# Performance work log

Hardware: AMD Instinct MI355X
Metric: run time of the kernel (lower is better)

Reference implementation:

```python
import jax, jax.numpy as jnp
import numpy as np
from jax.ops import segment_sum

N_NODES = 100000
N_EDGES = 1600000
N_GRAPHS = 64
IN_DIM = 128
HID = 128
N_CLASSES = 10


def setup_inputs() -> dict:
    key = jax.random.key(0)
    ks = jax.random.split(key, 8)
    h = jax.random.normal(ks[0], (N_NODES, IN_DIM), dtype=jnp.float32)
    src = jax.random.randint(ks[1], (N_EDGES,), 0, N_NODES, dtype=jnp.int64)
    dst = jax.random.randint(ks[2], (N_EDGES,), 0, N_NODES, dtype=jnp.int64)
    graph_ids = jnp.sort(jax.random.randint(ks[3], (N_NODES,), 0, N_GRAPHS, dtype=jnp.int64))
    # Glorot-ish scaled weights
    W1 = jax.random.normal(ks[4], (IN_DIM, HID), dtype=jnp.float32) / np.sqrt(IN_DIM)
    b1 = jnp.zeros((HID,), dtype=jnp.float32)
    W2 = jax.random.normal(ks[5], (HID, HID), dtype=jnp.float32) / np.sqrt(HID)
    b2 = jnp.zeros((HID,), dtype=jnp.float32)
    Wc = jax.random.normal(ks[6], (HID, N_CLASSES), dtype=jnp.float32) / np.sqrt(HID)
    bc = jnp.zeros((N_CLASSES,), dtype=jnp.float32)
    return {"h": h, "src": src, "dst": dst, "graph_ids": graph_ids,
            "W1": W1, "b1": b1, "W2": W2, "b2": b2, "Wc": Wc, "bc": bc}


def _graph_conv(h, src, dst, W, b, n_nodes):
    # DGL GraphConv, norm='both': D_out^{-1/2} scaling of src feats,
    # sum aggregation over edges, D_in^{-1/2} scaling of dst, then XW + b.
    ones = jnp.ones((src.shape[0],), dtype=h.dtype)
    deg_out = jnp.clip(segment_sum(ones, src, num_segments=n_nodes), 1.0)
    deg_in = jnp.clip(segment_sum(ones, dst, num_segments=n_nodes), 1.0)
    hn = h * jax.lax.rsqrt(deg_out)[:, None]          # [N, d]
    agg = segment_sum(hn[src], dst, num_segments=n_nodes)  # SpMM: [N, d]
    agg = agg * jax.lax.rsqrt(deg_in)[:, None]
    return agg @ W + b


def reference(h, src, dst, graph_ids, W1, b1, W2, b2, Wc, bc):
    n = h.shape[0]
    x = jax.nn.relu(_graph_conv(h, src, dst, W1, b1, n))
    x = jax.nn.relu(_graph_conv(x, src, dst, W2, b2, n))
    # mean_nodes readout per graph
    counts = jnp.clip(segment_sum(jnp.ones((n,), x.dtype), graph_ids, num_segments=N_GRAPHS), 1.0)
    hg = segment_sum(x, graph_ids, num_segments=N_GRAPHS) / counts[:, None]  # [G, d]
    return hg @ Wc + bc  # [G, n_classes]
```

## Files before the change

### kernel.cpp

```cpp
#include <hip/hip_runtime.h>

#define DIM 128
#define NG 64
#define NCLS 10
#define CAP 64
#define WSZ 256
#define NWMAX 512
#define CAPB 8192
#define EPB 8192
#define HL 4
#define WTP 68

typedef __attribute__((ext_vector_type(8))) short s8v;
typedef __attribute__((ext_vector_type(4))) float f4v;

__device__ inline unsigned short f2bf(float f) {
    unsigned int u = __float_as_uint(f);
    unsigned int r = (u + 0x7fffu + ((u >> 16) & 1u)) >> 16;
    return (unsigned short)r;
}
__device__ inline unsigned int pack2bf(float a, float b) {
    return ((unsigned int)f2bf(b) << 16) | (unsigned int)f2bf(a);
}

__global__ void prep_kernel(const float* __restrict__ W1, const float* __restrict__ W2,
                            unsigned short* __restrict__ Wt1, unsigned short* __restrict__ Wt2,
                            int* curD, int* curS, uint4* hb4, uint4* x1b4, int nw, int n) {
    int t = blockIdx.x * 256 + threadIdx.x;
    if (t < nw) {
        curD[t] = t * CAPB;
        curS[t] = t * CAPB;
    }
    if (t < 32768) {
        int which = t >> 14;
        int i = t & 16383;
        int c = i >> 7, k = i & 127;
        (which ? Wt2 : Wt1)[i] = f2bf((which ? W2 : W1)[k * 128 + c]);
    }
    if (t < 16) {
        uint4 z = make_uint4(0, 0, 0, 0);
        hb4[(size_t)n * 16 + t] = z;
        x1b4[(size_t)n * 16 + t] = z;
    }
}

__global__ __launch_bounds__(256) void bucket_kernel(const int* __restrict__ src,
                                                     const int* __restrict__ dst,
                                                     int* curD, int* curS,
                                                     int* __restrict__ bucketD,
                                                     unsigned char* __restrict__ bucketS,
                                                     int e, int nw) {
    __shared__ int histD[NWMAX];
    __shared__ int histS[NWMAX];
    int t = threadIdx.x;
    for (int i = t; i < nw; i += 256) { histD[i] = 0; histS[i] = 0; }
    __syncthreads();
    int lo = blockIdx.x * EPB;
    int hi = min(e, lo + EPB);
    for (int i = lo + t * 4; i < hi; i += 1024) {
        int4 d4 = *(const int4*)&dst[i];
        int4 s4 = *(const int4*)&src[i];
        atomicAdd(&histD[d4.x >> 8], 1); atomicAdd(&histS[s4.x >> 8], 1);
        atomicAdd(&histD[d4.y >> 8], 1); atomicAdd(&histS[s4.y >> 8], 1);
        atomicAdd(&histD[d4.z >> 8], 1); atomicAdd(&histS[s4.z >> 8], 1);
        atomicAdd(&histD[d4.w >> 8], 1); atomicAdd(&histS[s4.w >> 8], 1);
    }
    __syncthreads();
    for (int i = t; i < nw; i += 256) {
        int hd = histD[i], hs = histS[i];
        histD[i] = hd ? atomicAdd(&curD[i], hd) : 0;
        histS[i] = hs ? atomicAdd(&curS[i], hs) : 0;
    }
    __syncthreads();
    for (int i = lo + t * 4; i < hi; i += 1024) {
        int4 d4 = *(const int4*)&dst[i];
        int4 s4 = *(const int4*)&src[i];
#pragma unroll
        for (int j = 0; j < 4; ++j) {
            int d = (&d4.x)[j], s = (&s4.x)[j];
            int sd = atomicAdd(&histD[d >> 8], 1);
            bucketD[sd] = (s << 8) | (d & 255);
            int ss = atomicAdd(&histS[s >> 8], 1);
            bucketS[ss] = (unsigned char)(s & 255);
        }
    }
}

__global__ __launch_bounds__(256) void window_kernel(const int* __restrict__ curD,
                                                     const int* __restrict__ curS,
                                                     const int* __restrict__ bucketD,
                                                     const unsigned char* __restrict__ bucketS,
                                                     const float* __restrict__ h,
                                                     int* __restrict__ cnt_in,
                                                     float* __restrict__ rs_in,
                                                     float* __restrict__ rs_out,
                                                     int* __restrict__ colx_pad,
                                                     uint4* __restrict__ hb4, int n) {
    __shared__ int cin[WSZ];
    __shared__ int cout[WSZ];
    __shared__ float rsO_s[WSZ];
    int w = blockIdx.x, t = threadIdx.x;
    cin[t] = 0;
    cout[t] = 0;
    __syncthreads();
    int base = w * CAPB;
    int nE = min(curD[w] - base, CAPB);
    for (int i = t; i < nE; i += 256) {
        int v = bucketD[base + i];
        int d8 = v & 255;
        int slot = atomicAdd(&cin[d8], 1);
        if (slot < CAP) colx_pad[(((w << 8) + d8) << 6) + slot] = v >> 8;
    }
    int nS = min(curS[w] - base, CAPB);
    for (int i = t; i < nS; i += 256) atomicAdd(&cout[bucketS[base + i]], 1);
    __syncthreads();
    int node = (w << 8) + t;
    if (node < n) {
        int c = cin[t];
        cnt_in[node] = c;
        rs_in[node] = rsqrtf(fmaxf((float)c, 1.0f));
        float ro = rsqrtf(fmaxf((float)cout[t], 1.0f));
        rs_out[node] = ro;
        rsO_s[t] = ro;
        int cc = min(c, CAP);
        int c4 = min((cc + 3) & ~3, CAP);
        for (int s = cc; s < c4; ++s) colx_pad[((size_t)node << 6) + s] = n;
    }
    __syncthreads();
    for (int idx = t; idx < WSZ * 16; idx += 256) {
        int rl = idx >> 4, sub = idx & 15;
        int nd = (w << 8) + rl;
        if (nd < n) {
            float s = rsO_s[rl];
            float4 a = ((const float4*)h)[(size_t)nd * 32 + sub * 2];
            float4 b = ((const float4*)h)[(size_t)nd * 32 + sub * 2 + 1];
            uint4 o;
            o.x = pack2bf(a.x * s, a.y * s);
            o.y = pack2bf(a.z * s, a.w * s);
            o.z = pack2bf(b.x * s, b.y * s);
            o.w = pack2bf(b.z * s, b.w * s);
            hb4[(size_t)nd * 16 + sub] = o;
        }
    }
}

__global__ __launch_bounds__(256) void spmm_bf16(const uint4* __restrict__ xb4,
                                                 const int* __restrict__ cnt_in,
                                                 const int* __restrict__ colx_pad,
                                                 const float* __restrict__ rs_in,
                                                 uint4* __restrict__ yb4, int n) {
    int node = (blockIdx.x * 256 + threadIdx.x) >> 6;
    int lane = threadIdx.x & 63;
    if (node >= n) return;
    int g = lane >> 4, sub = lane & 15;
    int cnt = min(cnt_in[node], CAP);
    int cnt4 = min((cnt + 3) & ~3, CAP);
    int myc = colx_pad[((size_t)node << 6) + ((lane < cnt4) ? lane : 0)];
    float acc[8] = {0.f, 0.f, 0.f, 0.f, 0.f, 0.f, 0.f, 0.f};
    int j = 0;
    for (; j + 16 <= cnt4; j += 16) {
        uint4 v[4];
#pragma unroll
        for (int b = 0; b < 4; ++b) {
            int c = __shfl(myc, j + 4 * b + g);
            v[b] = xb4[(size_t)c * 16 + sub];
        }
#pragma unroll
        for (int b = 0; b < 4; ++b) {
            acc[0] += __uint_as_float(v[b].x << 16);
            acc[1] += __uint_as_float(v[b].x & 0xffff0000u);
            acc[2] += __uint_as_float(v[b].y << 16);
            acc[3] += __uint_as_float(v[b].y & 0xffff0000u);
            acc[4] += __uint_as_float(v[b].z << 16);
            acc[5] += __uint_as_float(v[b].z & 0xffff0000u);
            acc[6] += __uint_as_float(v[b].w << 16);
            acc[7] += __uint_as_float(v[b].w & 0xffff0000u);
        }
    }
    for (; j < cnt4; j += 4) {
        int c = __shfl(myc, j + g);
        uint4 v = xb4[(size_t)c * 16 + sub];
        acc[0] += __uint_as_float(v.x << 16);
        acc[1] += __uint_as_float(v.x & 0xffff0000u);
        acc[2] += __uint_as_float(v.y << 16);
        acc[3] += __uint_as_float(v.y & 0xffff0000u);
        acc[4] += __uint_as_float(v.z << 16);
        acc[5] += __uint_as_float(v.z & 0xffff0000u);
        acc[6] += __uint_as_float(v.w << 16);
        acc[7] += __uint_as_float(v.w & 0xffff0000u);
    }
#pragma unroll
    for (int i = 0; i < 8; ++i) {
        acc[i] += __shfl_xor(acc[i], 16);
        acc[i] += __shfl_xor(acc[i], 32);
    }
    if (g == 0) {
        float w = rs_in[node];
        uint4 o;
        o.x = pack2bf(acc[0] * w, acc[1] * w);
        o.y = pack2bf(acc[2] * w, acc[3] * w);
        o.z = pack2bf(acc[4] * w, acc[5] * w);
        o.w = pack2bf(acc[6] * w, acc[7] * w);
        yb4[(size_t)node * 16 + sub] = o;
    }
}

__device__ inline void stage_wt(const uint4* __restrict__ Wt4, unsigned int* WtL, int t) {
#pragma unroll
    for (int i = 0; i < 8; ++i) {
        int q = t + 256 * i;
        int row = q >> 4, col4 = q & 15;
        *(uint4*)&WtL[row * WTP + col4 * 4] = Wt4[q];
    }
}

__global__ __launch_bounds__(256) void mm_mfma(const unsigned char* __restrict__ A,
                                               const uint4* __restrict__ Wt4,
                                               const float* __restrict__ bias,
                                               const float* __restrict__ rs_out,
                                               unsigned short* __restrict__ out, int n) {
    __shared__ unsigned int WtL[128 * WTP];
    int t = threadIdx.x;
    stage_wt(Wt4, WtL, t);
    int wave = t >> 6, lane = t & 63;
    int m = lane & 15, q = lane >> 4;
    int r0 = (int)blockIdx.x * 64 + wave * 16;
    int arow = min(r0 + m, n - 1);
    __syncthreads();
    f4v acc[8];
#pragma unroll
    for (int c = 0; c < 8; ++c) acc[c] = (f4v){0.f, 0.f, 0.f, 0.f};
#pragma unroll
    for (int k0 = 0; k0 < 4; ++k0) {
        s8v a = *(const s8v*)(A + (size_t)arow * 256 + k0 * 64 + q * 16);
#pragma unroll
        for (int c = 0; c < 8; ++c) {
            s8v b = *(const s8v*)&WtL[(c * 16 + m) * WTP + k0 * 16 + q * 4];
            acc[c] = __builtin_amdgcn_mfma_f32_16x16x32_bf16(a, b, acc[c], 0, 0, 0);
        }
    }
#pragma unroll
    for (int c = 0; c < 8; ++c) {
        float bv = bias[c * 16 + m];
#pragma unroll
        for (int r = 0; r < 4; ++r) {
            int row = r0 + q * 4 + r;
            if (row < n) {
                float val = fmaxf(acc[c][r] + bv, 0.0f);
                out[(size_t)row * 128 + c * 16 + m] = f2bf(val * rs_out[row]);
            }
        }
    }
}

__global__ __launch_bounds__(256) void mm_mfma_readout(const unsigned char* __restrict__ A,
                                                       const uint4* __restrict__ Wt4,
                                                       const float* __restrict__ bias,
                                                       const int* __restrict__ gid,
                                                       float* __restrict__ hg, int n) {
    __shared__ unsigned int WtL[128 * WTP];
    __shared__ float hgloc[HL][DIM];
    int t = threadIdx.x;
    stage_wt(Wt4, WtL, t);
    for (int i = t; i < HL * DIM; i += 256) ((float*)hgloc)[i] = 0.0f;
    int wave = t >> 6, lane = t & 63;
    int m = lane & 15, q = lane >> 4;
    int r0 = (int)blockIdx.x * 64 + wave * 16;
    int b0 = (int)blockIdx.x * 64;
    int gid0 = gid[min(b0, n - 1)];
    int arow = min(r0 + m, n - 1);
    __syncthreads();
    f4v acc[8];
#pragma unroll
    for (int c = 0; c < 8; ++c) acc[c] = (f4v){0.f, 0.f, 0.f, 0.f};
#pragma unroll
    for (int k0 = 0; k0 < 4; ++k0) {
        s8v a = *(const s8v*)(A + (size_t)arow * 256 + k0 * 64 + q * 16);
#pragma unroll
        for (int c = 0; c < 8; ++c) {
            s8v b = *(const s8v*)&WtL[(c * 16 + m) * WTP + k0 * 16 + q * 4];
            acc[c] = __builtin_amdgcn_mfma_f32_16x16x32_bf16(a, b, acc[c], 0, 0, 0);
        }
    }
    int gfirst = gid[min(r0, n - 1)];
    int glast = gid[min(r0 + 15, n - 1)];
    bool uni = (gfirst == glast) && (r0 + 15 < n);
    if (uni) {
        int gl = gfirst - gid0;
#pragma unroll
        for (int c = 0; c < 8; ++c) {
            float bv = bias[c * 16 + m];
            float s = fmaxf(acc[c][0] + bv, 0.0f) + fmaxf(acc[c][1] + bv, 0.0f) +
                      fmaxf(acc[c][2] + bv, 0.0f) + fmaxf(acc[c][3] + bv, 0.0f);
            s += __shfl_xor(s, 16);
            s += __shfl_xor(s, 32);
            if (q == 0) {
                if (gl < HL)
                    atomicAdd(&hgloc[gl][c * 16 + m], s);
                else
                    atomicAdd(&hg[(size_t)gfirst * DIM + c * 16 + m], s);
            }
        }
    } else {
#pragma unroll
        for (int r = 0; r < 4; ++r) {
            int row = r0 + q * 4 + r;
            if (row < n) {
                int g = gid[row];
                int gl = g - gid0;
#pragma unroll
                for (int c = 0; c < 8; ++c) {
                    float val = fmaxf(acc[c][r] + bias[c * 16 + m], 0.0f);
                    if (gl < HL)
                        atomicAdd(&hgloc[gl][c * 16 + m], val);
                    else
                        atomicAdd(&hg[(size_t)g * DIM + c * 16 + m], val);
                }
            }
        }
    }
    __syncthreads();
    for (int i = t; i < HL * DIM; i += 256) {
        float v = ((float*)hgloc)[i];
        int g = gid0 + (i >> 7);
        if (v != 0.0f && g < NG) atomicAdd(&hg[(size_t)g * DIM + (i & 127)], v);
    }
}

__global__ void classify_kernel(const float* __restrict__ hg, const int* __restrict__ gid,
                                const float* __restrict__ Wc, const float* __restrict__ bc,
                                float* __restrict__ out, int n) {
    __shared__ float inv;
    int g = blockIdx.x, t = threadIdx.x;
    if (t == 0) {
        int lo = 0, hi = n;
        while (lo < hi) { int mid = (lo + hi) >> 1; if (gid[mid] < g) lo = mid + 1; else hi = mid; }
        int lb = lo;
        lo = 0; hi = n;
        while (lo < hi) { int mid = (lo + hi) >> 1; if (gid[mid] <= g) lo = mid + 1; else hi = mid; }
        inv = 1.0f / fmaxf((float)(lo - lb), 1.0f);
    }
    __syncthreads();
    if (t < NCLS) {
        float s = 0.0f;
        for (int k = 0; k < DIM; ++k) s = fmaf(hg[g * DIM + k], Wc[k * NCLS + t], s);
        out[g * NCLS + t] = s * inv + bc[t];
    }
}

extern "C" void kernel_launch(void* const* d_in, const int* in_sizes, int n_in,
                              void* d_out, int out_size, void* d_ws, size_t ws_size,
                              hipStream_t stream) {
    const float* h   = (const float*)d_in[0];
    const int*   src = (const int*)d_in[1];
    const int*   dst = (const int*)d_in[2];
    const int*   gid = (const int*)d_in[3];
    const float* W1  = (const float*)d_in[4];
    const float* b1  = (const float*)d_in[5];
    const float* W2  = (const float*)d_in[6];
    const float* b2  = (const float*)d_in[7];
    const float* Wc  = (const float*)d_in[8];
    const float* bc  = (const float*)d_in[9];
    float* out = (float*)d_out;

    const int n = in_sizes[0] / DIM;
    const int e = in_sizes[1];
    const int nw = (n + WSZ - 1) / WSZ;

    char* ws = (char*)d_ws;
    size_t off = 0;
    auto alloc = [&](size_t bytes) -> char* {
        char* p = ws + off;
        off = (off + bytes + 255) & ~(size_t)255;
        return p;
    };
    int*   cnt_in  = (int*)alloc((size_t)n * 4);
    float* rs_in   = (float*)alloc((size_t)n * 4);
    float* rs_out  = (float*)alloc((size_t)n * 4);
    int*   curD    = (int*)alloc((size_t)NWMAX * 4);
    int*   curS    = (int*)alloc((size_t)NWMAX * 4);
    int*   colx_pad = (int*)alloc((size_t)n * CAP * 4);
    int*   bucketD = (int*)alloc((size_t)nw * CAPB * 4);
    unsigned char* bucketS = (unsigned char*)alloc((size_t)nw * CAPB);
    float* hg      = (float*)alloc((size_t)NG * DIM * 4);
    unsigned short* Wt1 = (unsigned short*)alloc(128 * 128 * 2);
    unsigned short* Wt2 = (unsigned short*)alloc(128 * 128 * 2);
    uint4* hb4  = (uint4*)alloc((size_t)(n + 4) * 64 * 4);
    uint4* aggB = (uint4*)alloc((size_t)(n + 4) * 64 * 4);
    uint4* x1b4 = (uint4*)alloc((size_t)(n + 4) * 64 * 4);

    const int SPMM_B = (n + 3) / 4;
    const int MM_B = (n + 63) / 64;
    const int AB = (e + EPB - 1) / EPB;

    (void)hipMemsetAsync(hg, 0, (size_t)NG * DIM * 4, stream);

    prep_kernel<<<128, 256, 0, stream>>>(W1, W2, Wt1, Wt2, curD, curS, hb4, x1b4, nw, n);
    bucket_kernel<<<AB, 256, 0, stream>>>(src, dst, curD, curS, bucketD, bucketS, e, nw);
    window_kernel<<<nw, 256, 0, stream>>>(curD, curS, bucketD, bucketS, h,
                                          cnt_in, rs_in, rs_out, colx_pad, hb4, n);

    spmm_bf16<<<SPMM_B, 256, 0, stream>>>(hb4, cnt_in, colx_pad, rs_in, aggB, n);
    mm_mfma<<<MM_B, 256, 0, stream>>>((const unsigned char*)aggB, (const uint4*)Wt1,
                                      b1, rs_out, (unsigned short*)x1b4, n);
    spmm_bf16<<<SPMM_B, 256, 0, stream>>>(x1b4, cnt_in, colx_pad, rs_in, aggB, n);
    mm_mfma_readout<<<MM_B, 256, 0, stream>>>((const unsigned char*)aggB, (const uint4*)Wt2,
                                              b2, gid, hg, n);
    classify_kernel<<<NG, 64, 0, stream>>>(hg, gid, Wc, bc, out, n);
}
```

Before: 324.1 us.

## Fold hg memset into prep, enlarge bucket/window blocks, pad edges to 8

Zeroes the readout accumulator inside prep_kernel instead of a separate memset, removing one stream operation. Raises the bucket kernel to 1024 threads and the window kernel to 512 threads per block, so more threads work on each bucket's shared histogram. Pads each node's neighbour list to a multiple of 8 rather than 4, so the SpMM tail becomes a single two-load step instead of a serial loop. The wider padding adds gathers of the zero row.

```diff
diff --git a/kernel.cpp b/kernel.cpp
--- a/kernel.cpp
+++ b/kernel.cpp
@@ -25,7 +25,8 @@
 
 __global__ void prep_kernel(const float* __restrict__ W1, const float* __restrict__ W2,
                             unsigned short* __restrict__ Wt1, unsigned short* __restrict__ Wt2,
-                            int* curD, int* curS, uint4* hb4, uint4* x1b4, int nw, int n) {
+                            int* curD, int* curS, uint4* hb4, uint4* x1b4,
+                            float* __restrict__ hg, int nw, int n) {
     int t = blockIdx.x * 256 + threadIdx.x;
     if (t < nw) {
         curD[t] = t * CAPB;
@@ -37,6 +38,7 @@
         int c = i >> 7, k = i & 127;
         (which ? Wt2 : Wt1)[i] = f2bf((which ? W2 : W1)[k * 128 + c]);
     }
+    if (t < NG * DIM) hg[t] = 0.0f;
     if (t < 16) {
         uint4 z = make_uint4(0, 0, 0, 0);
         hb4[(size_t)n * 16 + t] = z;
@@ -44,20 +46,20 @@
     }
 }
 
-__global__ __launch_bounds__(256) void bucket_kernel(const int* __restrict__ src,
-                                                     const int* __restrict__ dst,
-                                                     int* curD, int* curS,
-                                                     int* __restrict__ bucketD,
-                                                     unsigned char* __restrict__ bucketS,
-                                                     int e, int nw) {
+__global__ __launch_bounds__(1024) void bucket_kernel(const int* __restrict__ src,
+                                                      const int* __restrict__ dst,
+                                                      int* curD, int* curS,
+                                                      int* __restrict__ bucketD,
+                                                      unsigned char* __restrict__ bucketS,
+                                                      int e, int nw) {
     __shared__ int histD[NWMAX];
     __shared__ int histS[NWMAX];
     int t = threadIdx.x;
-    for (int i = t; i < nw; i += 256) { histD[i] = 0; histS[i] = 0; }
+    for (int i = t; i < nw; i += 1024) { histD[i] = 0; histS[i] = 0; }
     __syncthreads();
     int lo = blockIdx.x * EPB;
     int hi = min(e, lo + EPB);
-    for (int i = lo + t * 4; i < hi; i += 1024) {
+    for (int i = lo + t * 4; i < hi; i += 4096) {
         int4 d4 = *(const int4*)&dst[i];
         int4 s4 = *(const int4*)&src[i];
         atomicAdd(&histD[d4.x >> 8], 1); atomicAdd(&histS[s4.x >> 8], 1);
@@ -66,13 +68,13 @@
         atomicAdd(&histD[d4.w >> 8], 1); atomicAdd(&histS[s4.w >> 8], 1);
     }
     __syncthreads();
-    for (int i = t; i < nw; i += 256) {
+    for (int i = t; i < nw; i += 1024) {
         int hd = histD[i], hs = histS[i];
         histD[i] = hd ? atomicAdd(&curD[i], hd) : 0;
         histS[i] = hs ? atomicAdd(&curS[i], hs) : 0;
     }
     __syncthreads();
-    for (int i = lo + t * 4; i < hi; i += 1024) {
+    for (int i = lo + t * 4; i < hi; i += 4096) {
         int4 d4 = *(const int4*)&dst[i];
         int4 s4 = *(const int4*)&src[i];
 #pragma unroll
@@ -86,7 +88,7 @@
     }
 }
 
-__global__ __launch_bounds__(256) void window_kernel(const int* __restrict__ curD,
+__global__ __launch_bounds__(512) void window_kernel(const int* __restrict__ curD,
                                                      const int* __restrict__ curS,
                                                      const int* __restrict__ bucketD,
                                                      const unsigned char* __restrict__ bucketS,
@@ -100,34 +102,35 @@
     __shared__ int cout[WSZ];
     __shared__ float rsO_s[WSZ];
     int w = blockIdx.x, t = threadIdx.x;
-    cin[t] = 0;
-    cout[t] = 0;
+    if (t < WSZ) { cin[t] = 0; cout[t] = 0; }
     __syncthreads();
     int base = w * CAPB;
     int nE = min(curD[w] - base, CAPB);
-    for (int i = t; i < nE; i += 256) {
+    for (int i = t; i < nE; i += 512) {
         int v = bucketD[base + i];
         int d8 = v & 255;
         int slot = atomicAdd(&cin[d8], 1);
         if (slot < CAP) colx_pad[(((w << 8) + d8) << 6) + slot] = v >> 8;
     }
     int nS = min(curS[w] - base, CAPB);
-    for (int i = t; i < nS; i += 256) atomicAdd(&cout[bucketS[base + i]], 1);
-    __syncthreads();
-    int node = (w << 8) + t;
-    if (node < n) {
-        int c = cin[t];
-        cnt_in[node] = c;
-        rs_in[node] = rsqrtf(fmaxf((float)c, 1.0f));
-        float ro = rsqrtf(fmaxf((float)cout[t], 1.0f));
-        rs_out[node] = ro;
-        rsO_s[t] = ro;
-        int cc = min(c, CAP);
-        int c4 = min((cc + 3) & ~3, CAP);
-        for (int s = cc; s < c4; ++s) colx_pad[((size_t)node << 6) + s] = n;
-    }
-    __syncthreads();
-    for (int idx = t; idx < WSZ * 16; idx += 256) {
+    for (int i = t; i < nS; i += 512) atomicAdd(&cout[bucketS[base + i]], 1);
+    __syncthreads();
+    if (t < WSZ) {
+        int node = (w << 8) + t;
+        if (node < n) {
+            int c = cin[t];
+            cnt_in[node] = c;
+            rs_in[node] = rsqrtf(fmaxf((float)c, 1.0f));
+            float ro = rsqrtf(fmaxf((float)cout[t], 1.0f));
+            rs_out[node] = ro;
+            rsO_s[t] = ro;
+            int cc = min(c, CAP);
+            int c8 = min((cc + 7) & ~7, CAP);
+            for (int s = cc; s < c8; ++s) colx_pad[((size_t)node << 6) + s] = n;
+        }
+    }
+    __syncthreads();
+    for (int idx = t; idx < WSZ * 16; idx += 512) {
         int rl = idx >> 4, sub = idx & 15;
         int nd = (w << 8) + rl;
         if (nd < n) {
@@ -154,11 +157,11 @@
     if (node >= n) return;
     int g = lane >> 4, sub = lane & 15;
     int cnt = min(cnt_in[node], CAP);
-    int cnt4 = min((cnt + 3) & ~3, CAP);
-    int myc = colx_pad[((size_t)node << 6) + ((lane < cnt4) ? lane : 0)];
+    int cnt8 = min((cnt + 7) & ~7, CAP);
+    int myc = colx_pad[((size_t)node << 6) + ((lane < cnt8) ? lane : 0)];
     float acc[8] = {0.f, 0.f, 0.f, 0.f, 0.f, 0.f, 0.f, 0.f};
     int j = 0;
-    for (; j + 16 <= cnt4; j += 16) {
+    for (; j + 16 <= cnt8; j += 16) {
         uint4 v[4];
 #pragma unroll
         for (int b = 0; b < 4; ++b) {
@@ -177,17 +180,23 @@
             acc[7] += __uint_as_float(v[b].w & 0xffff0000u);
         }
     }
-    for (; j < cnt4; j += 4) {
-        int c = __shfl(myc, j + g);
-        uint4 v = xb4[(size_t)c * 16 + sub];
-        acc[0] += __uint_as_float(v.x << 16);
-        acc[1] += __uint_as_float(v.x & 0xffff0000u);
-        acc[2] += __uint_as_float(v.y << 16);
-        acc[3] += __uint_as_float(v.y & 0xffff0000u);
-        acc[4] += __uint_as_float(v.z << 16);
-        acc[5] += __uint_as_float(v.z & 0xffff0000u);
-        acc[6] += __uint_as_float(v.w << 16);
-        acc[7] += __uint_as_float(v.w & 0xffff0000u);
+    if (j < cnt8) {
+        int c0 = __shfl(myc, j + g);
+        int c1 = __shfl(myc, j + 4 + g);
+        uint4 v0 = xb4[(size_t)c0 * 16 + sub];
+        uint4 v1 = xb4[(size_t)c1 * 16 + sub];
+#pragma unroll
+        for (int b = 0; b < 2; ++b) {
+            uint4 v = b ? v1 : v0;
+            acc[0] += __uint_as_float(v.x << 16);
+            acc[1] += __uint_as_float(v.x & 0xffff0000u);
+            acc[2] += __uint_as_float(v.y << 16);
+            acc[3] += __uint_as_float(v.y & 0xffff0000u);
+            acc[4] += __uint_as_float(v.z << 16);
+            acc[5] += __uint_as_float(v.z & 0xffff0000u);
+            acc[6] += __uint_as_float(v.w << 16);
+            acc[7] += __uint_as_float(v.w & 0xffff0000u);
+        }
     }
 #pragma unroll
     for (int i = 0; i < 8; ++i) {
@@ -393,11 +402,9 @@
     const int MM_B = (n + 63) / 64;
     const int AB = (e + EPB - 1) / EPB;
 
-    (void)hipMemsetAsync(hg, 0, (size_t)NG * DIM * 4, stream);
-
-    prep_kernel<<<128, 256, 0, stream>>>(W1, W2, Wt1, Wt2, curD, curS, hb4, x1b4, nw, n);
-    bucket_kernel<<<AB, 256, 0, stream>>>(src, dst, curD, curS, bucketD, bucketS, e, nw);
-    window_kernel<<<nw, 256, 0, stream>>>(curD, curS, bucketD, bucketS, h,
+    prep_kernel<<<128, 256, 0, stream>>>(W1, W2, Wt1, Wt2, curD, curS, hb4, x1b4, hg, nw, n);
+    bucket_kernel<<<AB, 1024, 0, stream>>>(src, dst, curD, curS, bucketD, bucketS, e, nw);
+    window_kernel<<<nw, 512, 0, stream>>>(curD, curS, bucketD, bucketS, h,
                                           cnt_in, rs_in, rs_out, colx_pad, hb4, n);
 
     spmm_bf16<<<SPMM_B, 256, 0, stream>>>(hb4, cnt_in, colx_pad, rs_in, aggB, n);
```

Result: faster. 309.4 us (-4.5%).
